# Optimization experiments

Measured on AMD Instinct MI355X. Metric: run time of the kernel, lower is better.

## Reference

```python
import jax, jax.numpy as jnp
import numpy as np

N, D, H = 6144, 768, 3
DH = D // H

def _lrelu(v):
    return jnp.where(v >= 0, v, 0.2 * v)

def setup_inputs() -> dict:
    key = jax.random.key(0)
    ks = jax.random.split(key, 8)
    s = 1.0 / np.sqrt(D)  # xavier-ish scale for D->D linears
    return {
        "x": jax.random.normal(ks[0], (N, D), dtype=jnp.float32),
        "adj_matrix": jax.random.randint(ks[1], (N, N), 0, 2, dtype=jnp.int32),
        "W_fc": jax.random.normal(ks[2], (D, D), dtype=jnp.float32) * s,
        "b_fc": jnp.zeros((D,), dtype=jnp.float32),
        "W_qfc": jax.random.normal(ks[3], (D, D), dtype=jnp.float32) * s,
        "b_qfc": jnp.zeros((D,), dtype=jnp.float32),
        "W_final": jax.random.normal(ks[4], (D, D), dtype=jnp.float32) * s,
        "b_final": jnp.zeros((D,), dtype=jnp.float32),
    }

def reference(x, adj_matrix, W_fc, b_fc, W_qfc, b_qfc, W_final, b_final):
    # x: [N, D], adj_matrix: [N, N] (0/1). Dropout is identity at eval.
    x_new = _lrelu(x @ W_fc.T + b_fc)          # [N, D]
    q = _lrelu(x_new @ W_qfc.T + b_qfc)        # [N, D]
    # torch.split(dim=2) into 3 contiguous chunks then cat on dim 0 == reshape heads
    xh = x_new.reshape(N, H, DH).transpose(1, 0, 2)   # [3, N, DH]
    qh = q.reshape(N, H, DH).transpose(1, 0, 2)       # [3, N, DH]
    scores = jnp.einsum('hnd,hmd->hnm', qh, xh) / 10.0  # [3, N, N]
    mask = (adj_matrix == 0)[None, :, :]                 # [1, N, N] -> broadcast
    scores = jnp.where(mask, -jnp.inf, scores)
    attn = jax.nn.softmax(scores, axis=-1)               # [3, N, N]
    out = jnp.einsum('hnm,hmd->hnd', attn, xh)           # [3, N, DH]
    out = out.transpose(1, 0, 2).reshape(N, D)           # cat heads on feature dim
    out = x + out                                        # residual 1
    ret = x + _lrelu(out @ W_final.T + b_final)          # residual 2
    return ret
```

## Files before the change

kernel.cpp:

```cpp
#include <hip/hip_runtime.h>
#include <stdint.h>

#define N_TOK 6144
#define DMODEL 768
#define NHEAD 3
#define DHEAD 256
#define NWORDS (N_TOK/32)
#define NT NWORDS

typedef __bf16 bf16x8 __attribute__((ext_vector_type(8)));
typedef float f32x4 __attribute__((ext_vector_type(4)));
typedef unsigned short u16;
typedef u16 u16x8 __attribute__((ext_vector_type(8)));
typedef u16 u16x4 __attribute__((ext_vector_type(4)));
typedef unsigned int u32;

__device__ __forceinline__ u16 f2bf(float f) {
  __bf16 b = (__bf16)f;
  return __builtin_bit_cast(u16, b);
}
__device__ __forceinline__ float bf2f(u16 u) {
  union { u32 u; float f; } v; v.u = (u32)u << 16; return v.f;
}
__device__ __forceinline__ float lrelu(float v) { return v >= 0.f ? v : 0.2f * v; }

__global__ __launch_bounds__(256) void cvt_bf(const float* __restrict__ src,
                                              u16* __restrict__ dst) {
  size_t i = ((size_t)blockIdx.x * 256 + threadIdx.x) * 8;
  float4 a = *reinterpret_cast<const float4*>(src + i);
  float4 b = *reinterpret_cast<const float4*>(src + i + 4);
  u16x8 v = {f2bf(a.x), f2bf(a.y), f2bf(a.z), f2bf(a.w),
             f2bf(b.x), f2bf(b.y), f2bf(b.z), f2bf(b.w)};
  *reinterpret_cast<u16x8*>(dst + i) = v;
}

__global__ __launch_bounds__(256) void pack_adj(const int* __restrict__ adj,
                                                u32* __restrict__ bits) {
  size_t wid = (size_t)blockIdx.x * 256 + threadIdx.x;
  const int4* p = reinterpret_cast<const int4*>(adj + wid * 32);
  u32 m = 0;
#pragma unroll
  for (int i = 0; i < 8; ++i) {
    int4 v = p[i];
    m |= (v.x != 0 ? 1u : 0u) << (i * 4 + 0);
    m |= (v.y != 0 ? 1u : 0u) << (i * 4 + 1);
    m |= (v.z != 0 ? 1u : 0u) << (i * 4 + 2);
    m |= (v.w != 0 ? 1u : 0u) << (i * 4 + 3);
  }
  bits[wid] = m;
}

__global__ __launch_bounds__(256) void transpose_bf(const u16* __restrict__ src,
                                                    u16* __restrict__ dst) {
  __shared__ u16 t[64][72];
  const int n0 = blockIdx.x * 64, d0 = blockIdx.y * 64;
  const int tid = threadIdx.x;
#pragma unroll
  for (int i = 0; i < 2; ++i) {
    int c = tid + i * 256;
    int r = c >> 3, c8 = (c & 7) * 8;
    *reinterpret_cast<u16x8*>(&t[r][c8]) =
        *reinterpret_cast<const u16x8*>(src + (size_t)(n0 + r) * DMODEL + d0 + c8);
  }
  __syncthreads();
#pragma unroll
  for (int i = 0; i < 2; ++i) {
    int c = tid + i * 256;
    int dr = c >> 3, n8 = (c & 7) * 8;
    u16x8 v;
#pragma unroll
    for (int j = 0; j < 8; ++j) v[j] = t[n8 + j][dr];
    *reinterpret_cast<u16x8*>(dst + (size_t)(d0 + dr) * N_TOK + n0 + n8) = v;
  }
}

__global__ void init_knmax(u32* knmax2) {
  if (threadIdx.x < NHEAD) knmax2[threadIdx.x] = 0;
}

__global__ __launch_bounds__(256) void knorm_max(const u16* __restrict__ xnew,
                                                 u32* __restrict__ knmax2) {
  int n = blockIdx.x * 256 + threadIdx.x;
  int h = blockIdx.y;
  const u16* row = xnew + (size_t)n * DMODEL + h * DHEAD;
  float s = 0.f;
#pragma unroll 4
  for (int i = 0; i < 32; ++i) {
    u16x8 v = *reinterpret_cast<const u16x8*>(row + i * 8);
#pragma unroll
    for (int j = 0; j < 8; ++j) { float f = bf2f(v[j]); s += f * f; }
  }
#pragma unroll
  for (int off = 1; off < 64; off <<= 1) s = fmaxf(s, __shfl_xor(s, off));
  if ((threadIdx.x & 63) == 0) atomicMax(knmax2 + h, __float_as_uint(s));
}

__global__ __launch_bounds__(256) void qbound(const u16* __restrict__ qbf,
                                              const u32* __restrict__ knmax2,
                                              float* __restrict__ Mrow) {
  int n = blockIdx.x * 256 + threadIdx.x;
  int h = blockIdx.y;
  const u16* row = qbf + (size_t)n * DMODEL + h * DHEAD;
  float s = 0.f;
#pragma unroll 4
  for (int i = 0; i < 32; ++i) {
    u16x8 v = *reinterpret_cast<const u16x8*>(row + i * 8);
#pragma unroll
    for (int j = 0; j < 8; ++j) { float f = bf2f(v[j]); s += f * f; }
  }
  float kn2 = __uint_as_float(knmax2[h]);
  Mrow[(size_t)h * N_TOK + n] = sqrtf(s * kn2);
}

template <int FINAL>
__global__ __launch_bounds__(256) void gemm_bf(const u16* __restrict__ A,
                                               const u16* __restrict__ W,
                                               const float* __restrict__ bias,
                                               const float* __restrict__ resid,
                                               u16* __restrict__ out_bf,
                                               float* __restrict__ out_f,
                                               float oscale) {
  __shared__ u16 As[128][72];
  __shared__ u16 Bs[128][72];
  const int tid = threadIdx.x;
  const int w = tid >> 6, lane = tid & 63, lr = lane & 15, lg = lane >> 4;
  const int m0 = blockIdx.x * 128, n0 = blockIdx.y * 128;
  const int wr = (w >> 1) * 64, wc = (w & 1) * 64;
  f32x4 acc[4][4] = {};
  u16x8 ast[4], bst[4];
  const int row = tid >> 3, c8 = (tid & 7) * 8;

  auto issue_tile = [&](int kt) {
#pragma unroll
    for (int i = 0; i < 4; ++i) {
      int r = row + i * 32;
      ast[i] = *reinterpret_cast<const u16x8*>(A + (size_t)(m0 + r) * DMODEL + kt * 64 + c8);
      bst[i] = *reinterpret_cast<const u16x8*>(W + (size_t)(n0 + r) * DMODEL + kt * 64 + c8);
    }
  };
  auto write_tile = [&]() {
#pragma unroll
    for (int i = 0; i < 4; ++i) {
      int r = row + i * 32;
      *reinterpret_cast<u16x8*>(&As[r][c8]) = ast[i];
      *reinterpret_cast<u16x8*>(&Bs[r][c8]) = bst[i];
    }
  };

  issue_tile(0);
  for (int kt = 0; kt < DMODEL / 64; ++kt) {
    __syncthreads();
    write_tile();
    if (kt + 1 < DMODEL / 64) issue_tile(kt + 1);
    __syncthreads();
#pragma unroll
    for (int ks = 0; ks < 2; ++ks) {
      bf16x8 a[4], b[4];
#pragma unroll
      for (int mi = 0; mi < 4; ++mi)
        a[mi] = *reinterpret_cast<const bf16x8*>(&As[wr + mi * 16 + lr][ks * 32 + lg * 8]);
#pragma unroll
      for (int ni = 0; ni < 4; ++ni)
        b[ni] = *reinterpret_cast<const bf16x8*>(&Bs[wc + ni * 16 + lr][ks * 32 + lg * 8]);
#pragma unroll
      for (int mi = 0; mi < 4; ++mi)
#pragma unroll
        for (int ni = 0; ni < 4; ++ni)
          acc[mi][ni] =
              __builtin_amdgcn_mfma_f32_16x16x32_bf16(a[mi], b[ni], acc[mi][ni], 0, 0, 0);
    }
  }
#pragma unroll
  for (int mi = 0; mi < 4; ++mi)
#pragma unroll
    for (int ni = 0; ni < 4; ++ni)
#pragma unroll
      for (int r = 0; r < 4; ++r) {
        int grow = m0 + wr + mi * 16 + lg * 4 + r;
        int gcol = n0 + wc + ni * 16 + lr;
        float v = lrelu(acc[mi][ni][r] + bias[gcol]);
        size_t idx = (size_t)grow * DMODEL + gcol;
        if (FINAL)
          out_f[idx] = resid[idx] + v;
        else
          out_bf[idx] = f2bf(v * oscale);
      }
}

template <int SPLIT>
__global__ __launch_bounds__(512) void attn_fused(
    const u16* __restrict__ Kmat,
    const u16* __restrict__ Qmat,
    const u16* __restrict__ VT,
    const u32* __restrict__ bits,
    const float* __restrict__ Mrow,
    const float* __restrict__ x,
    u16* __restrict__ out2,
    float* __restrict__ Opart,
    float* __restrict__ lpart) {
  __shared__ u16 Ks[32][264];
  __shared__ u16 Vs[256][36];
  __shared__ u16 Ps[8][16][40];
  __shared__ float lss[128];
  const int tid = threadIdx.x;
  const int w = tid >> 6, lane = tid & 63, lr = lane & 15, lg = lane >> 4;
  const int q0 = blockIdx.x * 128;
  const int h = blockIdx.y;
  const int z = blockIdx.z;
  const int qrow = q0 + w * 16 + lr;
  const int qp = (w >> 1) * 2;
  const int dbase = (w & 1) * 8;

  bf16x8 qf[8];
  {
    const u16* qrowp = Qmat + (size_t)qrow * DMODEL + h * DHEAD + lg * 8;
#pragma unroll
    for (int s = 0; s < 8; ++s) qf[s] = *reinterpret_cast<const bf16x8*>(qrowp + s * 32);
  }
  const float Mr = Mrow[(size_t)h * N_TOK + qrow];
  f32x4 o[2][8] = {};
  float lsum = 0.f;

  const int t0 = z * (NT / SPLIT), t1 = t0 + NT / SPLIT;

  u16x8 kst[2], vst[2];
  u32 wnext, wcur;

  auto issue_tile = [&](int kt) {
#pragma unroll
    for (int i = 0; i < 2; ++i) {
      int c = tid + i * 512;
      int kr = c >> 5, kc = (c & 31) * 8;
      kst[i] = *reinterpret_cast<const u16x8*>(
          Kmat + (size_t)(kt * 32 + kr) * DMODEL + h * DHEAD + kc);
      int vr = c >> 2, vc = (c & 3) * 8;
      vst[i] = *reinterpret_cast<const u16x8*>(
          VT + (size_t)(h * DHEAD + vr) * N_TOK + kt * 32 + vc);
    }
    wnext = bits[(size_t)qrow * NWORDS + kt];
  };
  auto write_tile = [&]() {
#pragma unroll
    for (int i = 0; i < 2; ++i) {
      int c = tid + i * 512;
      int kr = c >> 5, kc = (c & 31) * 8;
      *reinterpret_cast<u16x8*>(&Ks[kr][kc]) = kst[i];
      int vr = c >> 2, vc = (c & 3) * 8;
      *reinterpret_cast<u16x8*>(&Vs[vr][vc]) = vst[i];
    }
  };

  issue_tile(t0);

  for (int kt = t0; kt < t1; ++kt) {
    __syncthreads();
    write_tile();
    wcur = wnext;
    if (kt + 1 < t1) issue_tile(kt + 1);
    __syncthreads();

    f32x4 st[2] = {};
#pragma unroll
    for (int s = 0; s < 8; ++s) {
      bf16x8 k0 = *reinterpret_cast<const bf16x8*>(&Ks[lr][s * 32 + lg * 8]);
      bf16x8 k1 = *reinterpret_cast<const bf16x8*>(&Ks[16 + lr][s * 32 + lg * 8]);
      st[0] = __builtin_amdgcn_mfma_f32_16x16x32_bf16(k0, qf[s], st[0], 0, 0, 0);
      st[1] = __builtin_amdgcn_mfma_f32_16x16x32_bf16(k1, qf[s], st[1], 0, 0, 0);
    }
#pragma unroll
    for (int kb = 0; kb < 2; ++kb) {
      u16x4 pk;
#pragma unroll
      for (int r = 0; r < 4; ++r) {
        int keyl = kb * 16 + lg * 4 + r;
        float pe = ((wcur >> keyl) & 1u) ? __expf(st[kb][r] - Mr) : 0.f;
        lsum += pe;
        pk[r] = f2bf(pe);
      }
      *reinterpret_cast<u16x4*>(&Ps[w][lr][kb * 16 + lg * 4]) = pk;
    }
    __syncthreads();

    bf16x8 pf0 = *reinterpret_cast<const bf16x8*>(&Ps[qp][lr][lg * 8]);
    bf16x8 pf1 = *reinterpret_cast<const bf16x8*>(&Ps[qp + 1][lr][lg * 8]);
#pragma unroll
    for (int d = 0; d < 8; ++d) {
      bf16x8 vf = *reinterpret_cast<const bf16x8*>(&Vs[(dbase + d) * 16 + lr][lg * 8]);
      o[0][d] = __builtin_amdgcn_mfma_f32_16x16x32_bf16(pf0, vf, o[0][d], 0, 0, 0);
      o[1][d] = __builtin_amdgcn_mfma_f32_16x16x32_bf16(pf1, vf, o[1][d], 0, 0, 0);
    }
  }

  lsum += __shfl_xor(lsum, 16);
  lsum += __shfl_xor(lsum, 32);

  if (SPLIT == 1) {
    if (lane < 16) lss[w * 16 + lr] = lsum;
    __syncthreads();
#pragma unroll
    for (int t = 0; t < 2; ++t)
#pragma unroll
      for (int d = 0; d < 8; ++d)
#pragma unroll
        for (int r = 0; r < 4; ++r) {
          int grow = q0 + (w >> 1) * 32 + t * 16 + lg * 4 + r;
          int gcol = h * DHEAD + (w & 1) * 128 + d * 16 + lr;
          size_t idx = (size_t)grow * DMODEL + gcol;
          float ls = lss[(w >> 1) * 32 + t * 16 + lg * 4 + r];
          out2[idx] = f2bf(x[idx] + o[t][d][r] / ls);
        }
  } else {
    float* Op = Opart + (size_t)z * N_TOK * DMODEL;
#pragma unroll
    for (int t = 0; t < 2; ++t)
#pragma unroll
      for (int d = 0; d < 8; ++d)
#pragma unroll
        for (int r = 0; r < 4; ++r) {
          int grow = q0 + (w >> 1) * 32 + t * 16 + lg * 4 + r;
          int gcol = h * DHEAD + (w & 1) * 128 + d * 16 + lr;
          Op[(size_t)grow * DMODEL + gcol] = o[t][d][r];
        }
    if (lane < 16)
      lpart[((size_t)z * NHEAD + h) * N_TOK + qrow] = lsum;
  }
}

template <int SPLIT>
__global__ __launch_bounds__(256) void attn_combine(const float* __restrict__ Opart,
                                                    const float* __restrict__ lpart,
                                                    const float* __restrict__ x,
                                                    u16* __restrict__ out2) {
  int g = blockIdx.x * 256 + threadIdx.x;
  int q = g / (DMODEL / 4);
  int col = (g % (DMODEL / 4)) * 4;
  int h = col >> 8;
  float L = 0.f;
#pragma unroll
  for (int s = 0; s < SPLIT; ++s)
    L += lpart[((size_t)s * NHEAD + h) * N_TOK + q];
  float rL = 1.f / L;
  size_t idx = (size_t)q * DMODEL + col;
  float4 acc = make_float4(0.f, 0.f, 0.f, 0.f);
#pragma unroll
  for (int s = 0; s < SPLIT; ++s) {
    float4 O = *reinterpret_cast<const float4*>(Opart + (size_t)s * N_TOK * DMODEL + idx);
    acc.x += O.x; acc.y += O.y; acc.z += O.z; acc.w += O.w;
  }
  float4 xv = *reinterpret_cast<const float4*>(x + idx);
  u16x4 r;
  r[0] = f2bf(xv.x + acc.x * rL);
  r[1] = f2bf(xv.y + acc.y * rL);
  r[2] = f2bf(xv.z + acc.z * rL);
  r[3] = f2bf(xv.w + acc.w * rL);
  *reinterpret_cast<u16x4*>(out2 + idx) = r;
}

extern "C" void kernel_launch(void* const* d_in, const int* in_sizes, int n_in,
                              void* d_out, int out_size, void* d_ws, size_t ws_size,
                              hipStream_t stream) {
  const float* x     = (const float*)d_in[0];
  const int*   adj   = (const int*)d_in[1];
  const float* W_fc  = (const float*)d_in[2];
  const float* b_fc  = (const float*)d_in[3];
  const float* W_qfc = (const float*)d_in[4];
  const float* b_qfc = (const float*)d_in[5];
  const float* W_fin = (const float*)d_in[6];
  const float* b_fin = (const float*)d_in[7];
  float* out = (float*)d_out;

  char* ws = (char*)d_ws;
  size_t off = 0;
  auto alloc = [&](size_t bytes) {
    char* p = ws + off;
    off += (bytes + 255) & ~(size_t)255;
    return p;
  };
  u16* xnew_bf = (u16*)alloc((size_t)N_TOK * DMODEL * 2);
  u16* q_bf    = (u16*)alloc((size_t)N_TOK * DMODEL * 2);
  u16* xT      = (u16*)alloc((size_t)DMODEL * N_TOK * 2);
  u16* out2_bf = (u16*)alloc((size_t)N_TOK * DMODEL * 2);
  u16* x_bf    = (u16*)alloc((size_t)N_TOK * DMODEL * 2);
  u16* wfc_bf  = (u16*)alloc((size_t)DMODEL * DMODEL * 2);
  u16* wqf_bf  = (u16*)alloc((size_t)DMODEL * DMODEL * 2);
  u16* wfi_bf  = (u16*)alloc((size_t)DMODEL * DMODEL * 2);
  u32* bits    = (u32*)alloc((size_t)N_TOK * NWORDS * 4);
  u32* knmax2  = (u32*)alloc(NHEAD * 4);
  float* Mrow  = (float*)alloc((size_t)NHEAD * N_TOK * 4);
  size_t base_off = off;
  float* Opart = (float*)alloc((size_t)6 * N_TOK * DMODEL * 4);
  float* lpart = (float*)alloc((size_t)6 * NHEAD * N_TOK * 4);
  size_t need6 = off;
  auto needN = [&](size_t n) {
    return base_off + (((size_t)n * N_TOK * DMODEL * 4 + 255) & ~(size_t)255) +
           (((size_t)n * NHEAD * N_TOK * 4 + 255) & ~(size_t)255);
  };
  const int split = (ws_size >= need6) ? 6
                  : (ws_size >= needN(4)) ? 4
                  : (ws_size >= needN(2)) ? 2 : 1;

  cvt_bf<<<N_TOK * DMODEL / 8 / 256, 256, 0, stream>>>(x, x_bf);
  cvt_bf<<<DMODEL * DMODEL / 8 / 256, 256, 0, stream>>>(W_fc, wfc_bf);
  cvt_bf<<<DMODEL * DMODEL / 8 / 256, 256, 0, stream>>>(W_qfc, wqf_bf);
  cvt_bf<<<DMODEL * DMODEL / 8 / 256, 256, 0, stream>>>(W_fin, wfi_bf);
  pack_adj<<<N_TOK * NWORDS / 256, 256, 0, stream>>>(adj, bits);

  dim3 ggrid(N_TOK / 128, DMODEL / 128);
  gemm_bf<0><<<ggrid, 256, 0, stream>>>(x_bf, wfc_bf, b_fc, nullptr, xnew_bf, nullptr, 1.0f);
  gemm_bf<0><<<ggrid, 256, 0, stream>>>(xnew_bf, wqf_bf, b_qfc, nullptr, q_bf, nullptr,
                                        0.1f);
  transpose_bf<<<dim3(N_TOK / 64, DMODEL / 64), 256, 0, stream>>>(xnew_bf, xT);
  init_knmax<<<1, 64, 0, stream>>>(knmax2);
  dim3 bgrid(N_TOK / 256, NHEAD);
  knorm_max<<<bgrid, 256, 0, stream>>>(xnew_bf, knmax2);
  qbound<<<bgrid, 256, 0, stream>>>(q_bf, knmax2, Mrow);
  dim3 cgrid(N_TOK * DMODEL / 4 / 256);
  if (split == 6) {
    attn_fused<6><<<dim3(N_TOK / 128, NHEAD, 6), 512, 0, stream>>>(
        xnew_bf, q_bf, xT, bits, Mrow, x, out2_bf, Opart, lpart);
    attn_combine<6><<<cgrid, 256, 0, stream>>>(Opart, lpart, x, out2_bf);
  } else if (split == 4) {
    attn_fused<4><<<dim3(N_TOK / 128, NHEAD, 4), 512, 0, stream>>>(
        xnew_bf, q_bf, xT, bits, Mrow, x, out2_bf, Opart, lpart);
    attn_combine<4><<<cgrid, 256, 0, stream>>>(Opart, lpart, x, out2_bf);
  } else if (split == 2) {
    attn_fused<2><<<dim3(N_TOK / 128, NHEAD, 2), 512, 0, stream>>>(
        xnew_bf, q_bf, xT, bits, Mrow, x, out2_bf, Opart, lpart);
    attn_combine<2><<<cgrid, 256, 0, stream>>>(Opart, lpart, x, out2_bf);
  } else {
    attn_fused<1><<<dim3(N_TOK / 128, NHEAD, 1), 512, 0, stream>>>(
        xnew_bf, q_bf, xT, bits, Mrow, x, out2_bf, Opart, lpart);
  }
  gemm_bf<1><<<ggrid, 256, 0, stream>>>(out2_bf, wfi_bf, b_fin, x, nullptr, out, 1.0f);
}
```

Before: 361.1 us.

## Use 64-key tiles and 32x32x16 MFMA for the QK score product

```diff
diff --git a/kernel.cpp b/kernel.cpp
--- a/kernel.cpp
+++ b/kernel.cpp
@@ -6,10 +6,11 @@
 #define NHEAD 3
 #define DHEAD 256
 #define NWORDS (N_TOK/32)
-#define NT NWORDS
+#define NT64 (N_TOK/64)
 
 typedef __bf16 bf16x8 __attribute__((ext_vector_type(8)));
 typedef float f32x4 __attribute__((ext_vector_type(4)));
+typedef float f32x16 __attribute__((ext_vector_type(16)));
 typedef unsigned short u16;
 typedef u16 u16x8 __attribute__((ext_vector_type(8)));
 typedef u16 u16x4 __attribute__((ext_vector_type(4)));
@@ -198,54 +199,56 @@
     u16* __restrict__ out2,
     float* __restrict__ Opart,
     float* __restrict__ lpart) {
-  __shared__ u16 Ks[32][264];
-  __shared__ u16 Vs[256][36];
-  __shared__ u16 Ps[8][16][40];
-  __shared__ float lss[128];
+  __shared__ u16 Ks[64][264];
+  __shared__ u16 Vs[256][72];
+  __shared__ u16 Ps[4][32][72];
+  __shared__ float lss[2][128];
   const int tid = threadIdx.x;
-  const int w = tid >> 6, lane = tid & 63, lr = lane & 15, lg = lane >> 4;
+  const int w = tid >> 6, lane = tid & 63;
+  const int g = w >> 1, kh = w & 1;
+  const int ll = lane & 31, hi = lane >> 5;
+  const int lr = lane & 15, lg = lane >> 4;
   const int q0 = blockIdx.x * 128;
   const int h = blockIdx.y;
   const int z = blockIdx.z;
-  const int qrow = q0 + w * 16 + lr;
-  const int qp = (w >> 1) * 2;
-  const int dbase = (w & 1) * 8;
-
-  bf16x8 qf[8];
+  const int qrow = q0 + g * 32 + ll;
+  const int dhb = kh * 8;
+
+  bf16x8 qf[16];
   {
-    const u16* qrowp = Qmat + (size_t)qrow * DMODEL + h * DHEAD + lg * 8;
-#pragma unroll
-    for (int s = 0; s < 8; ++s) qf[s] = *reinterpret_cast<const bf16x8*>(qrowp + s * 32);
+    const u16* qp = Qmat + (size_t)qrow * DMODEL + h * DHEAD + hi * 8;
+#pragma unroll
+    for (int s = 0; s < 16; ++s) qf[s] = *reinterpret_cast<const bf16x8*>(qp + s * 16);
   }
   const float Mr = Mrow[(size_t)h * N_TOK + qrow];
   f32x4 o[2][8] = {};
   float lsum = 0.f;
 
-  const int t0 = z * (NT / SPLIT), t1 = t0 + NT / SPLIT;
-
-  u16x8 kst[2], vst[2];
+  const int t0 = z * (NT64 / SPLIT), t1 = t0 + NT64 / SPLIT;
+
+  u16x8 kst[4], vst[4];
   u32 wnext, wcur;
 
   auto issue_tile = [&](int kt) {
 #pragma unroll
-    for (int i = 0; i < 2; ++i) {
+    for (int i = 0; i < 4; ++i) {
       int c = tid + i * 512;
       int kr = c >> 5, kc = (c & 31) * 8;
       kst[i] = *reinterpret_cast<const u16x8*>(
-          Kmat + (size_t)(kt * 32 + kr) * DMODEL + h * DHEAD + kc);
-      int vr = c >> 2, vc = (c & 3) * 8;
+          Kmat + (size_t)(kt * 64 + kr) * DMODEL + h * DHEAD + kc);
+      int vr = c >> 3, vc = (c & 7) * 8;
       vst[i] = *reinterpret_cast<const u16x8*>(
-          VT + (size_t)(h * DHEAD + vr) * N_TOK + kt * 32 + vc);
-    }
-    wnext = bits[(size_t)qrow * NWORDS + kt];
+          VT + (size_t)(h * DHEAD + vr) * N_TOK + kt * 64 + vc);
+    }
+    wnext = bits[(size_t)qrow * NWORDS + kt * 2 + kh];
   };
   auto write_tile = [&]() {
 #pragma unroll
-    for (int i = 0; i < 2; ++i) {
+    for (int i = 0; i < 4; ++i) {
       int c = tid + i * 512;
       int kr = c >> 5, kc = (c & 31) * 8;
       *reinterpret_cast<u16x8*>(&Ks[kr][kc]) = kst[i];
-      int vr = c >> 2, vc = (c & 3) * 8;
+      int vr = c >> 3, vc = (c & 7) * 8;
       *reinterpret_cast<u16x8*>(&Vs[vr][vc]) = vst[i];
     }
   };
@@ -259,54 +262,56 @@
     if (kt + 1 < t1) issue_tile(kt + 1);
     __syncthreads();
 
-    f32x4 st[2] = {};
-#pragma unroll
-    for (int s = 0; s < 8; ++s) {
-      bf16x8 k0 = *reinterpret_cast<const bf16x8*>(&Ks[lr][s * 32 + lg * 8]);
-      bf16x8 k1 = *reinterpret_cast<const bf16x8*>(&Ks[16 + lr][s * 32 + lg * 8]);
-      st[0] = __builtin_amdgcn_mfma_f32_16x16x32_bf16(k0, qf[s], st[0], 0, 0, 0);
-      st[1] = __builtin_amdgcn_mfma_f32_16x16x32_bf16(k1, qf[s], st[1], 0, 0, 0);
-    }
-#pragma unroll
-    for (int kb = 0; kb < 2; ++kb) {
+    f32x16 st = {};
+#pragma unroll
+    for (int s = 0; s < 16; ++s) {
+      bf16x8 kf = *reinterpret_cast<const bf16x8*>(&Ks[kh * 32 + ll][s * 16 + hi * 8]);
+      st = __builtin_amdgcn_mfma_f32_32x32x16_bf16(kf, qf[s], st, 0, 0, 0);
+    }
+#pragma unroll
+    for (int rg = 0; rg < 4; ++rg) {
       u16x4 pk;
 #pragma unroll
-      for (int r = 0; r < 4; ++r) {
-        int keyl = kb * 16 + lg * 4 + r;
-        float pe = ((wcur >> keyl) & 1u) ? __expf(st[kb][r] - Mr) : 0.f;
+      for (int j = 0; j < 4; ++j) {
+        int keyl = rg * 8 + 4 * hi + j;
+        float pe = ((wcur >> keyl) & 1u) ? __expf(st[rg * 4 + j] - Mr) : 0.f;
         lsum += pe;
-        pk[r] = f2bf(pe);
+        pk[j] = f2bf(pe);
       }
-      *reinterpret_cast<u16x4*>(&Ps[w][lr][kb * 16 + lg * 4]) = pk;
+      *reinterpret_cast<u16x4*>(&Ps[g][ll][kh * 32 + rg * 8 + hi * 4]) = pk;
     }
     __syncthreads();
 
-    bf16x8 pf0 = *reinterpret_cast<const bf16x8*>(&Ps[qp][lr][lg * 8]);
-    bf16x8 pf1 = *reinterpret_cast<const bf16x8*>(&Ps[qp + 1][lr][lg * 8]);
-#pragma unroll
-    for (int d = 0; d < 8; ++d) {
-      bf16x8 vf = *reinterpret_cast<const bf16x8*>(&Vs[(dbase + d) * 16 + lr][lg * 8]);
-      o[0][d] = __builtin_amdgcn_mfma_f32_16x16x32_bf16(pf0, vf, o[0][d], 0, 0, 0);
-      o[1][d] = __builtin_amdgcn_mfma_f32_16x16x32_bf16(pf1, vf, o[1][d], 0, 0, 0);
-    }
-  }
-
-  lsum += __shfl_xor(lsum, 16);
+#pragma unroll
+    for (int ks = 0; ks < 2; ++ks) {
+      bf16x8 pf0 = *reinterpret_cast<const bf16x8*>(&Ps[g][lr][ks * 32 + lg * 8]);
+      bf16x8 pf1 = *reinterpret_cast<const bf16x8*>(&Ps[g][16 + lr][ks * 32 + lg * 8]);
+#pragma unroll
+      for (int d = 0; d < 8; ++d) {
+        bf16x8 vf = *reinterpret_cast<const bf16x8*>(
+            &Vs[(dhb + d) * 16 + lr][ks * 32 + lg * 8]);
+        o[0][d] = __builtin_amdgcn_mfma_f32_16x16x32_bf16(pf0, vf, o[0][d], 0, 0, 0);
+        o[1][d] = __builtin_amdgcn_mfma_f32_16x16x32_bf16(pf1, vf, o[1][d], 0, 0, 0);
+      }
+    }
+  }
+
   lsum += __shfl_xor(lsum, 32);
+  if (lane < 32) lss[kh][g * 32 + lane] = lsum;
+  __syncthreads();
 
   if (SPLIT == 1) {
-    if (lane < 16) lss[w * 16 + lr] = lsum;
-    __syncthreads();
 #pragma unroll
     for (int t = 0; t < 2; ++t)
 #pragma unroll
       for (int d = 0; d < 8; ++d)
 #pragma unroll
         for (int r = 0; r < 4; ++r) {
-          int grow = q0 + (w >> 1) * 32 + t * 16 + lg * 4 + r;
-          int gcol = h * DHEAD + (w & 1) * 128 + d * 16 + lr;
+          int gq = g * 32 + t * 16 + lg * 4 + r;
+          float ls = lss[0][gq] + lss[1][gq];
+          int grow = q0 + gq;
+          int gcol = h * DHEAD + kh * 128 + d * 16 + lr;
           size_t idx = (size_t)grow * DMODEL + gcol;
-          float ls = lss[(w >> 1) * 32 + t * 16 + lg * 4 + r];
           out2[idx] = f2bf(x[idx] + o[t][d][r] / ls);
         }
   } else {
@@ -317,12 +322,14 @@
       for (int d = 0; d < 8; ++d)
 #pragma unroll
         for (int r = 0; r < 4; ++r) {
-          int grow = q0 + (w >> 1) * 32 + t * 16 + lg * 4 + r;
-          int gcol = h * DHEAD + (w & 1) * 128 + d * 16 + lr;
+          int grow = q0 + g * 32 + t * 16 + lg * 4 + r;
+          int gcol = h * DHEAD + kh * 128 + d * 16 + lr;
           Op[(size_t)grow * DMODEL + gcol] = o[t][d][r];
         }
-    if (lane < 16)
-      lpart[((size_t)z * NHEAD + h) * N_TOK + qrow] = lsum;
+    if (kh == 0 && lane < 32) {
+      int gq = g * 32 + lane;
+      lpart[((size_t)z * NHEAD + h) * N_TOK + q0 + gq] = lss[0][gq] + lss[1][gq];
+    }
   }
 }
 
```

Measured after the change: 339.7 us. 5.9% less time.
